# Kernel tuning notes

Hardware: AMD Instinct MI355X
Metric: run time of the kernel (lower is better)

## Reference

```python
import jax, jax.numpy as jnp
import numpy as np

N_TOK, D_MODEL, N_EXPERTS, TOP_K = 8192, 512, 8, 2


def setup_inputs() -> dict:
    key = jax.random.key(0)
    k1, k2, k3 = jax.random.split(key, 3)
    x = jax.random.normal(k1, (N_TOK, D_MODEL), jnp.float32)
    w_gate = jax.random.normal(k2, (D_MODEL, N_EXPERTS), jnp.float32) * 0.02
    expert_w = jax.random.normal(k3, (N_EXPERTS, D_MODEL, D_MODEL), jnp.float32) * (D_MODEL ** -0.5)
    return {"x": x, "w_gate": w_gate, "expert_w": expert_w, "top_k": TOP_K}


def _cv_sq(v):
    m = jnp.mean(v)
    return jnp.var(v) / (m * m + 1e-10)


def reference(x, w_gate, expert_w, top_k):
    # ---- Gate (clean top-k gating, eval mode of noisy-top-k) ----
    logits = x @ w_gate                              # [N, E]
    top_vals, top_idx = jax.lax.top_k(logits, top_k)  # [N, k]
    top_gates = jax.nn.softmax(top_vals, axis=-1)
    n, e = logits.shape
    gates = jnp.zeros((n, e), x.dtype).at[jnp.arange(n)[:, None], top_idx].set(top_gates)

    # ---- dispatch -> per-expert GEMM -> log-domain combine ----
    # combine(): stitched = cat(expert_out).exp() * nonzero_gates; index_add over
    # batch index; zeros -> eps; log. Dense-equivalent (tokens with gate 0
    # contribute exactly nothing):
    expert_out = jnp.einsum('nd,edf->nef', x, expert_w)   # per-expert outputs [N, E, D]
    combined = jnp.einsum('ne,nef->nf', gates, jnp.exp(expert_out))  # [N, D]
    eps = np.float32(np.finfo(np.float64).eps)
    combined = jnp.where(combined == 0, eps, combined)
    out = jnp.log(combined)

    # ---- load-balance aux loss: cv^2(importance) + cv^2(load) ----
    importance = gates.sum(0)
    load = (gates > 0).sum(0).astype(x.dtype)
    balance_loss = _cv_sq(importance) + _cv_sq(load)
    return out, balance_loss
```

## Files before the change

### kernel.cpp

```cpp
#include <hip/hip_runtime.h>
#include <hip/hip_bf16.h>
#include <math.h>

#define N_TOK 8192
#define D 512
#define NE 8

typedef float f32x4 __attribute__((ext_vector_type(4)));
typedef __bf16 bf16x8 __attribute__((ext_vector_type(8)));
typedef unsigned short u16;
typedef u16 u16x8 __attribute__((ext_vector_type(8)));

#define OFF_TOKE  256
#define OFF_TOKG  65792
#define OFF_BUCK  131328
#define OFF_XB    (1u << 20)
#define OFF_EWT   (OFF_XB + 8u * 1024 * 1024)
#define OFF_Y     (OFF_EWT + 4u * 1024 * 1024)

__device__ __forceinline__ u16 f2b(float v) {
    __hip_bfloat16 h = __float2bfloat16(v);
    return *reinterpret_cast<u16*>(&h);
}
__device__ __forceinline__ float b2f(u16 u) {
    __hip_bfloat16 h;
    *reinterpret_cast<u16*>(&h) = u;
    return __bfloat162float(h);
}

typedef __attribute__((address_space(1))) const void* gp1_t;
typedef __attribute__((address_space(3))) void* lp3_t;
__device__ __forceinline__ void gload16(const void* g, void* l) {
    __builtin_amdgcn_global_load_lds((gp1_t)g, (lp3_t)l, 16, 0, 0);
}

__global__ __launch_bounds__(256) void gate_prep_kernel(
    const float* __restrict__ x, const float* __restrict__ wg,
    const float* __restrict__ ew,
    int* __restrict__ tok_e, float* __restrict__ tok_g, u16* __restrict__ xb,
    u16* __restrict__ ewt)
{
    __shared__ __align__(16) float sbuf[64 * 65];
    int b = blockIdx.x;
    int tid = threadIdx.x;

    if (b >= 2048) {
        int pb = b - 2048;
        float (*tile)[65] = (float(*)[65])sbuf;
        int e = pb >> 6, dt = (pb >> 3) & 7, ftl = pb & 7;
        int c = tid & 63, rq = tid >> 6;
        const float* src = ew + (size_t)e * D * D + (size_t)(dt * 64) * D + ftl * 64;
#pragma unroll
        for (int i = 0; i < 16; ++i) {
            int r = i * 4 + rq;
            tile[r][c] = src[(size_t)r * D + c];
        }
        __syncthreads();
        u16* dst = ewt + (size_t)e * D * D + (size_t)(ftl * 64) * D + dt * 64;
#pragma unroll
        for (int i = 0; i < 16; ++i) {
            int f = i * 4 + rq;
            dst[(size_t)f * D + c] = f2b(tile[c][f]);
        }
        return;
    }

    float* wgs = sbuf;
    for (int i = tid; i < NE * D; i += 256) {
        int d = i >> 3, e = i & 7;
        wgs[e * D + d] = wg[i];
    }
    __syncthreads();

    int wave = tid >> 6, lane = tid & 63;
    int n = b * 4 + wave;
    const float* xr = x + (size_t)n * D;
    u16* xbr = xb + (size_t)n * D;

    float p[NE];
#pragma unroll
    for (int e = 0; e < NE; ++e) p[e] = 0.f;
#pragma unroll
    for (int it = 0; it < 8; ++it) {
        float xv = xr[it * 64 + lane];
        xbr[it * 64 + lane] = f2b(xv);
#pragma unroll
        for (int e = 0; e < NE; ++e)
            p[e] += xv * wgs[e * D + it * 64 + lane];
    }
#pragma unroll
    for (int off = 32; off > 0; off >>= 1) {
#pragma unroll
        for (int e = 0; e < NE; ++e)
            p[e] += __shfl_xor(p[e], off);
    }

    if (lane == 0) {
        int e1 = 0; float v1 = p[0];
#pragma unroll
        for (int e = 1; e < NE; ++e) if (p[e] > v1) { v1 = p[e]; e1 = e; }
        int e2 = -1; float v2 = -INFINITY;
#pragma unroll
        for (int e = 0; e < NE; ++e) if (e != e1 && p[e] > v2) { v2 = p[e]; e2 = e; }
        float t = __expf(v2 - v1);
        float inv = 1.f / (1.f + t);
        tok_e[2 * n] = e1;     tok_e[2 * n + 1] = e2;
        tok_g[2 * n] = inv;    tok_g[2 * n + 1] = t * inv;
    }
}

__global__ __launch_bounds__(256) void bucketize_kernel(
    const int* __restrict__ tok_e, const float* __restrict__ tok_g,
    int* __restrict__ count, float* __restrict__ imp, int* __restrict__ bucket)
{
    __shared__ int lcnt[NE], lbase[NE];
    __shared__ float limp[NE];
    int tid = threadIdx.x;
    if (tid < NE) { lcnt[tid] = 0; limp[tid] = 0.f; }
    __syncthreads();

    int n = blockIdx.x * 256 + tid;
    int e1 = tok_e[2 * n], e2 = tok_e[2 * n + 1];
    float g1 = tok_g[2 * n], g2 = tok_g[2 * n + 1];
    int o1 = atomicAdd(&lcnt[e1], 1);
    int o2 = atomicAdd(&lcnt[e2], 1);
    atomicAdd(&limp[e1], g1);
    atomicAdd(&limp[e2], g2);
    __syncthreads();
    if (tid < NE) {
        lbase[tid] = atomicAdd(&count[tid], lcnt[tid]);
        atomicAdd(&imp[tid], limp[tid]);
    }
    __syncthreads();
    bucket[e1 * N_TOK + lbase[e1] + o1] = 2 * n;
    bucket[e2 * N_TOK + lbase[e2] + o2] = 2 * n + 1;
}

__global__ __launch_bounds__(256) void moe_gemm(
    const u16* __restrict__ xb, const u16* __restrict__ ewt,
    const int* __restrict__ count, const int* __restrict__ bucket,
    u16* __restrict__ y)
{
    int b = blockIdx.x;
    int ft = b & 3;
    int tt = (b >> 2) & 63;
    int e  = b >> 8;
    int cnt = count[e];
    if (tt * 128 >= cnt) return;

    __shared__ int sl[128];
    __shared__ __align__(16) u16 smem[32768];

    int tid = threadIdx.x;
    if (tid < 128) {
        int idx = tt * 128 + tid;
        sl[tid] = (idx < cnt) ? bucket[e * N_TOK + idx] : -1;
    }
    __syncthreads();

    int w = tid >> 6, l = tid & 63;
    int c8 = (l & 3) * 8;
    int r0 = w * 32 + (l >> 2);
    int r1 = r0 + 16;
    int s0 = sl[r0], s1 = sl[r1];
    int ta0 = (s0 < 0) ? 0 : (s0 >> 1);
    int ta1 = (s1 < 0) ? 0 : (s1 >> 1);
    const u16* gA0 = xb + (size_t)ta0 * D + c8;
    const u16* gA1 = xb + (size_t)ta1 * D + c8;
    const u16* gB0 = ewt + ((size_t)e * D + ft * 128 + r0) * D + c8;
    const u16* gB1 = ewt + ((size_t)e * D + ft * 128 + r1) * D + c8;
    int wo = w * 1024;

    int wm = w & 1, wn = w >> 1;
    int lm = l & 15, quad = l >> 4, kq = quad * 8;

    f32x4 acc[4][4] = {};

    {
        u16* nb = smem;
        gload16(gA0, nb + wo);
        gload16(gA1, nb + wo + 512);
        gload16(gB0, nb + 8192 + wo);
        gload16(gB1, nb + 8192 + wo + 512);
    }

    for (int kc = 0; kc < 16; ++kc) {
        __syncthreads();
        if (kc < 15) {
            u16* nb = smem + ((kc + 1) & 1) * 16384;
            gload16(gA0 + (kc + 1) * 32, nb + wo);
            gload16(gA1 + (kc + 1) * 32, nb + wo + 512);
            gload16(gB0 + (kc + 1) * 32, nb + 8192 + wo);
            gload16(gB1 + (kc + 1) * 32, nb + 8192 + wo + 512);
        }
        const u16* As = smem + (kc & 1) * 16384;
        const u16* Bs = As + 8192;

        bf16x8 af[4], bfv[4];
#pragma unroll
        for (int i = 0; i < 4; ++i)
            af[i] = *(const bf16x8*)&As[(wm * 64 + i * 16 + lm) * 32 + kq];
#pragma unroll
        for (int j = 0; j < 4; ++j)
            bfv[j] = *(const bf16x8*)&Bs[(wn * 64 + j * 16 + lm) * 32 + kq];
#pragma unroll
        for (int i = 0; i < 4; ++i)
#pragma unroll
            for (int j = 0; j < 4; ++j)
                acc[i][j] = __builtin_amdgcn_mfma_f32_16x16x32_bf16(
                    af[i], bfv[j], acc[i][j], 0, 0, 0);
    }

    __syncthreads();
    u16* Es = smem + w * 2304;
#pragma unroll
    for (int h = 0; h < 2; ++h) {
#pragma unroll
        for (int i2 = 0; i2 < 2; ++i2) {
            int i = h * 2 + i2;
#pragma unroll
            for (int j = 0; j < 4; ++j)
#pragma unroll
                for (int r = 0; r < 4; ++r)
                    Es[(i2 * 16 + quad * 4 + r) * 72 + j * 16 + lm] =
                        f2b(acc[i][j][r]);
        }
        int row = l >> 1, hc = l & 1;
        int s = sl[wm * 64 + h * 32 + row];
        const u16* src = Es + row * 72 + hc * 32;
        u16* dst = y + (size_t)((s < 0) ? 0 : s) * D + ft * 128 + wn * 64 + hc * 32;
        if (s >= 0) {
#pragma unroll
            for (int c = 0; c < 4; ++c)
                *(u16x8*)(dst + c * 8) = *(const u16x8*)(src + c * 8);
        }
    }
}

__global__ __launch_bounds__(256) void combine_kernel(
    const u16* __restrict__ y, const float* __restrict__ tok_g,
    const int* __restrict__ count, const float* __restrict__ imp,
    float* __restrict__ out)
{
    if (blockIdx.x == 2048) {
        if (threadIdx.x == 0) {
            float mi = 0.f, ml = 0.f;
            for (int e = 0; e < NE; ++e) { mi += imp[e]; ml += (float)count[e]; }
            mi *= 0.125f; ml *= 0.125f;
            float vi = 0.f, vl = 0.f;
            for (int e = 0; e < NE; ++e) {
                float di = imp[e] - mi;          vi += di * di;
                float dl = (float)count[e] - ml; vl += dl * dl;
            }
            vi *= 0.125f; vl *= 0.125f;
            out[N_TOK * D] = vi / (mi * mi + 1e-10f) + vl / (ml * ml + 1e-10f);
        }
        return;
    }
    int idx = blockIdx.x * 256 + threadIdx.x;
    int n = idx >> 6;
    int c = (idx & 63) * 8;
    const u16x8 ua = *(const u16x8*)(y + (size_t)(2 * n) * D + c);
    const u16x8 ub = *(const u16x8*)(y + (size_t)(2 * n + 1) * D + c);
    float g1 = tok_g[2 * n], g2 = tok_g[2 * n + 1];
    const float eps = 2.2204460492503131e-16f;
    float r[8];
#pragma unroll
    for (int i = 0; i < 8; ++i) {
        float v = g1 * __expf(b2f(ua[i])) + g2 * __expf(b2f(ub[i]));
        r[i] = __logf(v == 0.f ? eps : v);
    }
    float* o = out + (size_t)n * D + c;
    *(float4*)(o)     = *(float4*)&r[0];
    *(float4*)(o + 4) = *(float4*)&r[4];
}

extern "C" void kernel_launch(void* const* d_in, const int* in_sizes, int n_in,
                              void* d_out, int out_size, void* d_ws, size_t ws_size,
                              hipStream_t stream)
{
    const float* x  = (const float*)d_in[0];
    const float* wg = (const float*)d_in[1];
    const float* ew = (const float*)d_in[2];
    char* ws = (char*)d_ws;
    int*   count  = (int*)(ws + 0);
    float* imp    = (float*)(ws + 64);
    int*   tok_e  = (int*)(ws + OFF_TOKE);
    float* tok_g  = (float*)(ws + OFF_TOKG);
    int*   bucket = (int*)(ws + OFF_BUCK);
    u16*   xb     = (u16*)(ws + OFF_XB);
    u16*   ewt    = (u16*)(ws + OFF_EWT);
    u16*   y      = (u16*)(ws + OFF_Y);
    float* out    = (float*)d_out;

    hipMemsetAsync(ws, 0, 128, stream);
    gate_prep_kernel<<<2048 + 512, 256, 0, stream>>>(x, wg, ew, tok_e, tok_g, xb, ewt);
    bucketize_kernel<<<N_TOK / 256, 256, 0, stream>>>(tok_e, tok_g, count, imp, bucket);
    moe_gemm<<<NE * 64 * 4, 256, 0, stream>>>(xb, ewt, count, bucket, y);
    combine_kernel<<<2049, 256, 0, stream>>>(y, tok_g, count, imp, out);
}
```

Measured before the change: 128.0 us.

## Shrink MoE GEMM token tile to 64 and drop LDS double buffering

The token tile per block drops from 128 to 64 rows and the grid doubles, so there are more blocks to spread across CUs. Accumulators per wave halve and LDS use falls from about 64KB to about 18KB, which should allow more resident blocks per CU and cut padding waste on each expert's last tile. The double-buffered prefetch is replaced by a single buffer with load-sync-compute on every k step. That exposes global-load latency, which the extra occupancy has to hide, and B tiles are now re-read twice as often.

```diff
diff --git a/kernel.cpp b/kernel.cpp
--- a/kernel.cpp
+++ b/kernel.cpp
@@ -143,68 +143,54 @@
 {
     int b = blockIdx.x;
     int ft = b & 3;
-    int tt = (b >> 2) & 63;
-    int e  = b >> 8;
+    int tt = (b >> 2) & 127;
+    int e  = b >> 9;
     int cnt = count[e];
-    if (tt * 128 >= cnt) return;
-
-    __shared__ int sl[128];
-    __shared__ __align__(16) u16 smem[32768];
+    if (tt * 64 >= cnt) return;
+
+    __shared__ int sl[64];
+    __shared__ __align__(16) u16 smem[9216];
 
     int tid = threadIdx.x;
-    if (tid < 128) {
-        int idx = tt * 128 + tid;
+    if (tid < 64) {
+        int idx = tt * 64 + tid;
         sl[tid] = (idx < cnt) ? bucket[e * N_TOK + idx] : -1;
     }
     __syncthreads();
 
     int w = tid >> 6, l = tid & 63;
     int c8 = (l & 3) * 8;
-    int r0 = w * 32 + (l >> 2);
-    int r1 = r0 + 16;
-    int s0 = sl[r0], s1 = sl[r1];
-    int ta0 = (s0 < 0) ? 0 : (s0 >> 1);
-    int ta1 = (s1 < 0) ? 0 : (s1 >> 1);
-    const u16* gA0 = xb + (size_t)ta0 * D + c8;
-    const u16* gA1 = xb + (size_t)ta1 * D + c8;
-    const u16* gB0 = ewt + ((size_t)e * D + ft * 128 + r0) * D + c8;
-    const u16* gB1 = ewt + ((size_t)e * D + ft * 128 + r1) * D + c8;
-    int wo = w * 1024;
+    int ra = w * 16 + (l >> 2);
+    int sa = sl[ra];
+    const u16* gA = xb + (size_t)((sa < 0) ? 0 : (sa >> 1)) * D + c8;
+    u16* lA = &smem[w * 512];
+    int fb0 = w * 32 + (l >> 2);
+    const u16* gB0 = ewt + ((size_t)e * D + ft * 128 + fb0) * D + c8;
+    const u16* gB1 = gB0 + (size_t)16 * D;
+    u16* lB0 = &smem[2048 + w * 1024];
+    u16* lB1 = lB0 + 512;
 
     int wm = w & 1, wn = w >> 1;
     int lm = l & 15, quad = l >> 4, kq = quad * 8;
 
-    f32x4 acc[4][4] = {};
-
-    {
-        u16* nb = smem;
-        gload16(gA0, nb + wo);
-        gload16(gA1, nb + wo + 512);
-        gload16(gB0, nb + 8192 + wo);
-        gload16(gB1, nb + 8192 + wo + 512);
-    }
+    f32x4 acc[2][4] = {};
 
     for (int kc = 0; kc < 16; ++kc) {
         __syncthreads();
-        if (kc < 15) {
-            u16* nb = smem + ((kc + 1) & 1) * 16384;
-            gload16(gA0 + (kc + 1) * 32, nb + wo);
-            gload16(gA1 + (kc + 1) * 32, nb + wo + 512);
-            gload16(gB0 + (kc + 1) * 32, nb + 8192 + wo);
-            gload16(gB1 + (kc + 1) * 32, nb + 8192 + wo + 512);
-        }
-        const u16* As = smem + (kc & 1) * 16384;
-        const u16* Bs = As + 8192;
-
-        bf16x8 af[4], bfv[4];
-#pragma unroll
-        for (int i = 0; i < 4; ++i)
-            af[i] = *(const bf16x8*)&As[(wm * 64 + i * 16 + lm) * 32 + kq];
+        gload16(gA + kc * 32, lA);
+        gload16(gB0 + kc * 32, lB0);
+        gload16(gB1 + kc * 32, lB1);
+        __syncthreads();
+
+        bf16x8 af[2], bfv[4];
+#pragma unroll
+        for (int i = 0; i < 2; ++i)
+            af[i] = *(const bf16x8*)&smem[(wm * 32 + i * 16 + lm) * 32 + kq];
 #pragma unroll
         for (int j = 0; j < 4; ++j)
-            bfv[j] = *(const bf16x8*)&Bs[(wn * 64 + j * 16 + lm) * 32 + kq];
-#pragma unroll
-        for (int i = 0; i < 4; ++i)
+            bfv[j] = *(const bf16x8*)&smem[2048 + (wn * 64 + j * 16 + lm) * 32 + kq];
+#pragma unroll
+        for (int i = 0; i < 2; ++i)
 #pragma unroll
             for (int j = 0; j < 4; ++j)
                 acc[i][j] = __builtin_amdgcn_mfma_f32_16x16x32_bf16(
@@ -214,26 +200,21 @@
     __syncthreads();
     u16* Es = smem + w * 2304;
 #pragma unroll
-    for (int h = 0; h < 2; ++h) {
-#pragma unroll
-        for (int i2 = 0; i2 < 2; ++i2) {
-            int i = h * 2 + i2;
-#pragma unroll
-            for (int j = 0; j < 4; ++j)
-#pragma unroll
-                for (int r = 0; r < 4; ++r)
-                    Es[(i2 * 16 + quad * 4 + r) * 72 + j * 16 + lm] =
-                        f2b(acc[i][j][r]);
-        }
-        int row = l >> 1, hc = l & 1;
-        int s = sl[wm * 64 + h * 32 + row];
-        const u16* src = Es + row * 72 + hc * 32;
-        u16* dst = y + (size_t)((s < 0) ? 0 : s) * D + ft * 128 + wn * 64 + hc * 32;
-        if (s >= 0) {
-#pragma unroll
-            for (int c = 0; c < 4; ++c)
-                *(u16x8*)(dst + c * 8) = *(const u16x8*)(src + c * 8);
-        }
+    for (int i = 0; i < 2; ++i)
+#pragma unroll
+        for (int j = 0; j < 4; ++j)
+#pragma unroll
+            for (int r = 0; r < 4; ++r)
+                Es[(i * 16 + quad * 4 + r) * 72 + j * 16 + lm] =
+                    f2b(acc[i][j][r]);
+    int row = l >> 1, hc = l & 1;
+    int s = sl[wm * 32 + row];
+    const u16* src = Es + row * 72 + hc * 32;
+    u16* dst = y + (size_t)((s < 0) ? 0 : s) * D + ft * 128 + wn * 64 + hc * 32;
+    if (s >= 0) {
+#pragma unroll
+        for (int c = 0; c < 4; ++c)
+            *(u16x8*)(dst + c * 8) = *(const u16x8*)(src + c * 8);
     }
 }
 
@@ -296,6 +277,6 @@
     hipMemsetAsync(ws, 0, 128, stream);
     gate_prep_kernel<<<2048 + 512, 256, 0, stream>>>(x, wg, ew, tok_e, tok_g, xb, ewt);
     bucketize_kernel<<<N_TOK / 256, 256, 0, stream>>>(tok_e, tok_g, count, imp, bucket);
-    moe_gemm<<<NE * 64 * 4, 256, 0, stream>>>(xb, ewt, count, bucket, y);
+    moe_gemm<<<NE * 128 * 4, 256, 0, stream>>>(xb, ewt, count, bucket, y);
     combine_kernel<<<2049, 256, 0, stream>>>(y, tok_g, count, imp, out);
 }
```

Result: no change. 127.9 us (-0.1%).

## Replace double-buffered K loop with single-buffered 64-wide K chunks

Applied to the files above, without the earlier changes.

The GEMM main loop drops its two-stage shared-memory double buffer. Each iteration now loads a 64-wide K chunk into a single buffer, synchronises, and then runs two MFMA sub-steps. Shared memory per block is halved, which may let more blocks share a CU, and there are half as many loop iterations and barriers. In exchange, global-to-LDS loads no longer overlap with MFMA compute inside a block, so latency hiding relies on other resident waves.

```diff
diff --git a/kernel.cpp b/kernel.cpp
--- a/kernel.cpp
+++ b/kernel.cpp
@@ -149,7 +149,7 @@
     if (tt * 128 >= cnt) return;
 
     __shared__ int sl[128];
-    __shared__ __align__(16) u16 smem[32768];
+    __shared__ __align__(16) u16 smem[16384];
 
     int tid = threadIdx.x;
     if (tid < 128) {
@@ -163,52 +163,54 @@
     int r0 = w * 32 + (l >> 2);
     int r1 = r0 + 16;
     int s0 = sl[r0], s1 = sl[r1];
-    int ta0 = (s0 < 0) ? 0 : (s0 >> 1);
-    int ta1 = (s1 < 0) ? 0 : (s1 >> 1);
-    const u16* gA0 = xb + (size_t)ta0 * D + c8;
-    const u16* gA1 = xb + (size_t)ta1 * D + c8;
+    const u16* gA0 = xb + (size_t)((s0 < 0) ? 0 : (s0 >> 1)) * D + c8;
+    const u16* gA1 = xb + (size_t)((s1 < 0) ? 0 : (s1 >> 1)) * D + c8;
     const u16* gB0 = ewt + ((size_t)e * D + ft * 128 + r0) * D + c8;
     const u16* gB1 = ewt + ((size_t)e * D + ft * 128 + r1) * D + c8;
-    int wo = w * 1024;
+    u16* lA0 = &smem[w * 1024 + l * 8];
+    u16* lA1 = &smem[w * 1024 + 512 + l * 8];
+    u16* lB0 = &smem[8192 + w * 1024 + l * 8];
+    u16* lB1 = &smem[8192 + w * 1024 + 512 + l * 8];
 
     int wm = w & 1, wn = w >> 1;
     int lm = l & 15, quad = l >> 4, kq = quad * 8;
 
     f32x4 acc[4][4] = {};
 
-    {
-        u16* nb = smem;
-        gload16(gA0, nb + wo);
-        gload16(gA1, nb + wo + 512);
-        gload16(gB0, nb + 8192 + wo);
-        gload16(gB1, nb + 8192 + wo + 512);
-    }
-
-    for (int kc = 0; kc < 16; ++kc) {
+    for (int kc = 0; kc < 8; ++kc) {
+        const u16* pA0 = gA0 + kc * 64;
+        const u16* pA1 = gA1 + kc * 64;
+        const u16* pB0 = gB0 + kc * 64;
+        const u16* pB1 = gB1 + kc * 64;
         __syncthreads();
-        if (kc < 15) {
-            u16* nb = smem + ((kc + 1) & 1) * 16384;
-            gload16(gA0 + (kc + 1) * 32, nb + wo);
-            gload16(gA1 + (kc + 1) * 32, nb + wo + 512);
-            gload16(gB0 + (kc + 1) * 32, nb + 8192 + wo);
-            gload16(gB1 + (kc + 1) * 32, nb + 8192 + wo + 512);
-        }
-        const u16* As = smem + (kc & 1) * 16384;
-        const u16* Bs = As + 8192;
-
-        bf16x8 af[4], bfv[4];
-#pragma unroll
-        for (int i = 0; i < 4; ++i)
-            af[i] = *(const bf16x8*)&As[(wm * 64 + i * 16 + lm) * 32 + kq];
-#pragma unroll
-        for (int j = 0; j < 4; ++j)
-            bfv[j] = *(const bf16x8*)&Bs[(wn * 64 + j * 16 + lm) * 32 + kq];
-#pragma unroll
-        for (int i = 0; i < 4; ++i)
+        gload16(pA0,      lA0);
+        gload16(pA1,      lA1);
+        gload16(pA0 + 32, lA0 + 4096);
+        gload16(pA1 + 32, lA1 + 4096);
+        gload16(pB0,      lB0);
+        gload16(pB1,      lB1);
+        gload16(pB0 + 32, lB0 + 4096);
+        gload16(pB1 + 32, lB1 + 4096);
+        __syncthreads();
+
+#pragma unroll
+        for (int ks = 0; ks < 2; ++ks) {
+            const u16* As = smem + ks * 4096;
+            const u16* Bs = smem + 8192 + ks * 4096;
+            bf16x8 af[4], bfv[4];
+#pragma unroll
+            for (int i = 0; i < 4; ++i)
+                af[i] = *(const bf16x8*)&As[(wm * 64 + i * 16 + lm) * 32 + kq];
 #pragma unroll
             for (int j = 0; j < 4; ++j)
-                acc[i][j] = __builtin_amdgcn_mfma_f32_16x16x32_bf16(
-                    af[i], bfv[j], acc[i][j], 0, 0, 0);
+                bfv[j] = *(const bf16x8*)&Bs[(wn * 64 + j * 16 + lm) * 32 + kq];
+#pragma unroll
+            for (int i = 0; i < 4; ++i)
+#pragma unroll
+                for (int j = 0; j < 4; ++j)
+                    acc[i][j] = __builtin_amdgcn_mfma_f32_16x16x32_bf16(
+                        af[i], bfv[j], acc[i][j], 0, 0, 0);
+        }
     }
 
     __syncthreads();
```

Result: faster. 124.0 us (-3.1%).
